# Kernel optimization log

Measured on AMD Instinct MI355X. Metric: run time of the kernel, lower is better.

Reference implementation:

```python
import jax, jax.numpy as jnp
import numpy as np

P = 256         # ids_per_batch
K = 16          # imgs_per_id
D = 2048        # feature_dim
MARGIN = 10.0
EPS = 1e-12


def setup_inputs() -> dict:
    key = jax.random.key(0)
    features = jax.random.normal(key, (P * K, D), dtype=jnp.float32)
    # ordered batch: label i repeated K times, matching targets[0::imgs_per_id] slicing
    targets = jnp.repeat(jnp.arange(P, dtype=jnp.int64), K)
    return {"features": features, "targets": targets}


def reference(features, targets):
    # ordered path: batch == P*K, labels grouped -> reshape replaces the per-class python loop
    f = features.reshape(P, K, D)               # [P, K, D]
    centers = f.mean(axis=1)                    # [P, D] per-class mean

    # intra: euclidean dist from each center to its own K features, max per class
    intra_d2 = jnp.sum((f - centers[:, None, :]) ** 2, axis=-1)     # [P, K]
    intra_max = jnp.max(jnp.sqrt(jnp.clip(intra_d2, EPS, None)), axis=1)  # [P]

    # inter: pairwise center distances, min over other centers
    cc = jnp.sum(centers ** 2, axis=1)                              # [P]
    cd2 = cc[:, None] + cc[None, :] - 2.0 * (centers @ centers.T)   # [P, P]
    cd = jnp.sqrt(jnp.clip(cd2, EPS, None))
    cd = jnp.where(jnp.eye(P, dtype=bool), jnp.inf, cd)             # exclude self
    inter_min = jnp.min(cd, axis=1)                                 # [P]

    cluster_loss = jnp.mean(jax.nn.relu(intra_max - inter_min + MARGIN))
    return cluster_loss, intra_max, inter_min
```

## Files before the change

### kernel.cpp

```cpp
#include <hip/hip_runtime.h>
#include <math.h>

#define NP 256
#define NK 16
#define ND 2048
#define MARGIN 10.0f
#define EPSV 1e-12f

__global__ __launch_bounds__(256) void k_center_intra(
    const float* __restrict__ F, float* __restrict__ centers,
    float* __restrict__ cc, float* __restrict__ out) {
  const int p = blockIdx.x;
  const int t = threadIdx.x;

  float acc[NK];
#pragma unroll
  for (int k = 0; k < NK; ++k) acc[k] = 0.f;
  float ccp = 0.f;

#pragma unroll
  for (int j = 0; j < 2; ++j) {
    const int dbase = j * 1024 + t * 4;
    float4 x[NK];
#pragma unroll
    for (int k = 0; k < NK; ++k)
      x[k] = *reinterpret_cast<const float4*>(
          &F[((size_t)(p * NK + k)) * ND + dbase]);
    float4 c;
    c.x = c.y = c.z = c.w = 0.f;
#pragma unroll
    for (int k = 0; k < NK; ++k) {
      c.x += x[k].x; c.y += x[k].y; c.z += x[k].z; c.w += x[k].w;
    }
    const float inv = 1.0f / 16.0f;
    c.x *= inv; c.y *= inv; c.z *= inv; c.w *= inv;
    *reinterpret_cast<float4*>(&centers[(size_t)p * ND + dbase]) = c;
    ccp += c.x * c.x + c.y * c.y + c.z * c.z + c.w * c.w;
#pragma unroll
    for (int k = 0; k < NK; ++k) {
      float dx = x[k].x - c.x, dy = x[k].y - c.y;
      float dz = x[k].z - c.z, dw = x[k].w - c.w;
      acc[k] += dx * dx + dy * dy + dz * dz + dw * dw;
    }
  }

#pragma unroll
  for (int k = 0; k < NK; ++k) {
    float v = acc[k];
#pragma unroll
    for (int m = 32; m > 0; m >>= 1) v += __shfl_xor(v, m);
    acc[k] = v;
  }
  {
    float v = ccp;
#pragma unroll
    for (int m = 32; m > 0; m >>= 1) v += __shfl_xor(v, m);
    ccp = v;
  }

  __shared__ float red[4][NK + 1];
  const int wave = t >> 6, lane = t & 63;
  if (lane == 0) {
#pragma unroll
    for (int k = 0; k < NK; ++k) red[wave][k] = acc[k];
    red[wave][NK] = ccp;
  }
  __syncthreads();
  if (t == 0) {
    float m = 0.f;
#pragma unroll
    for (int k = 0; k < NK; ++k) {
      float s = red[0][k] + red[1][k] + red[2][k] + red[3][k];
      m = fmaxf(m, sqrtf(fmaxf(s, EPSV)));
    }
    out[1 + p] = m;
    cc[p] = red[0][NK] + red[1][NK] + red[2][NK] + red[3][NK];
  }
}

#define BK 128
#define LDP 132

__global__ __launch_bounds__(256) void k_gemm(
    const float* __restrict__ C, float* __restrict__ G) {
  __shared__ float As[64][LDP];
  __shared__ float Bs[64][LDP];
  const int t = threadIdx.x;
  const int p0 = blockIdx.x * 64;
  const int q0 = blockIdx.y * 64;
  const int k0 = blockIdx.z * BK;

#pragma unroll
  for (int rep = 0; rep < 8; ++rep) {
    const int idx = rep * 256 + t;
    const int r = idx >> 5;
    const int c4 = idx & 31;
    float4 a = *reinterpret_cast<const float4*>(
        &C[(size_t)(p0 + r) * ND + k0 + c4 * 4]);
    float4 b = *reinterpret_cast<const float4*>(
        &C[(size_t)(q0 + r) * ND + k0 + c4 * 4]);
    *reinterpret_cast<float4*>(&As[r][c4 * 4]) = a;
    *reinterpret_cast<float4*>(&Bs[r][c4 * 4]) = b;
  }
  __syncthreads();

  const int ti = t >> 4;
  const int tj = t & 15;
  float acc[4][4] = {};

#pragma unroll
  for (int kk = 0; kk < BK; kk += 4) {
    float4 a4[4], b4[4];
#pragma unroll
    for (int u = 0; u < 4; ++u)
      a4[u] = *reinterpret_cast<const float4*>(&As[ti + u * 16][kk]);
#pragma unroll
    for (int v = 0; v < 4; ++v)
      b4[v] = *reinterpret_cast<const float4*>(&Bs[tj + v * 16][kk]);
#pragma unroll
    for (int u = 0; u < 4; ++u)
#pragma unroll
      for (int v = 0; v < 4; ++v)
        acc[u][v] += a4[u].x * b4[v].x + a4[u].y * b4[v].y +
                     a4[u].z * b4[v].z + a4[u].w * b4[v].w;
  }

#pragma unroll
  for (int u = 0; u < 4; ++u)
#pragma unroll
    for (int v = 0; v < 4; ++v)
      atomicAdd(&G[(size_t)(p0 + ti + u * 16) * NP + q0 + tj + v * 16],
                acc[u][v]);
}

__global__ __launch_bounds__(256) void k_inter(
    const float* __restrict__ G, const float* __restrict__ cc,
    float* __restrict__ out) {
  const int p = blockIdx.x, q = threadIdx.x;
  const float g = G[(size_t)p * NP + q];
  const float cd2 = cc[p] + cc[q] - 2.0f * g;
  float cd = (q == p) ? INFINITY : sqrtf(fmaxf(cd2, EPSV));
#pragma unroll
  for (int m = 32; m > 0; m >>= 1) cd = fminf(cd, __shfl_xor(cd, m));
  __shared__ float red[4];
  if ((q & 63) == 0) red[q >> 6] = cd;
  __syncthreads();
  if (q == 0)
    out[1 + NP + p] =
        fminf(fminf(red[0], red[1]), fminf(red[2], red[3]));
}

__global__ __launch_bounds__(256) void k_loss(float* __restrict__ out) {
  const int t = threadIdx.x;
  const float im = out[1 + t];
  const float in_ = out[1 + NP + t];
  float v = fmaxf(im - in_ + MARGIN, 0.f);
#pragma unroll
  for (int m = 32; m > 0; m >>= 1) v += __shfl_xor(v, m);
  __shared__ float red[4];
  if ((t & 63) == 0) red[t >> 6] = v;
  __syncthreads();
  if (t == 0) out[0] = (red[0] + red[1] + red[2] + red[3]) / (float)NP;
}

extern "C" void kernel_launch(void* const* d_in, const int* in_sizes, int n_in,
                              void* d_out, int out_size, void* d_ws,
                              size_t ws_size, hipStream_t stream) {
  const float* F = (const float*)d_in[0];
  float* out = (float*)d_out;

  float* centers = (float*)d_ws;
  float* cc = centers + (size_t)NP * ND;
  float* G = cc + NP;

  hipMemsetAsync(G, 0, (size_t)NP * NP * sizeof(float), stream);
  k_center_intra<<<NP, 256, 0, stream>>>(F, centers, cc, out);
  k_gemm<<<dim3(4, 4, 16), 256, 0, stream>>>(centers, G);
  k_inter<<<NP, 256, 0, stream>>>(G, cc, out);
  k_loss<<<1, 256, 0, stream>>>(out);
}
```

Measured before the change: 34.79 us.

## Use bf16 MFMA for center Gram matrix and fuse inter-min via atomicMin

Centers are stored as bf16, and the Gram matrix is computed with 16x16x32 bf16 MFMA instructions. The pairwise distance and min reduction are fused into the GEMM epilogue using an integer atomicMin on non-negative floats, which drops the memset, the split-K atomics and the separate inter kernel. The center kernel now uses 512 threads per block, one d-chunk per thread, and initialises the inter-min output to infinity. The bf16 rounding of centers costs precision in the cd2 cancellation, which could perturb inter_min values.

New measurement: 35.07 us. Within noise of the previous version (+0.8%).

```diff
diff --git a/kernel.cpp b/kernel.cpp
--- a/kernel.cpp
+++ b/kernel.cpp
@@ -7,41 +7,48 @@
 #define MARGIN 10.0f
 #define EPSV 1e-12f
 
-__global__ __launch_bounds__(256) void k_center_intra(
-    const float* __restrict__ F, float* __restrict__ centers,
+typedef short bf16x8 __attribute__((ext_vector_type(8)));
+typedef float f32x4 __attribute__((ext_vector_type(4)));
+
+static __device__ __forceinline__ unsigned short f2bf(float f) {
+  unsigned u = __float_as_uint(f);
+  unsigned r = (u + 0x7fffu + ((u >> 16) & 1u)) >> 16;
+  return (unsigned short)r;
+}
+
+__global__ __launch_bounds__(512) void k_center_intra(
+    const float* __restrict__ F, unsigned short* __restrict__ Cb,
     float* __restrict__ cc, float* __restrict__ out) {
   const int p = blockIdx.x;
   const int t = threadIdx.x;
+  const int d = t * 4;
+
+  float4 x[NK];
+#pragma unroll
+  for (int k = 0; k < NK; ++k)
+    x[k] = *reinterpret_cast<const float4*>(&F[((size_t)(p * NK + k)) * ND + d]);
+
+  float4 c;
+  c.x = c.y = c.z = c.w = 0.f;
+#pragma unroll
+  for (int k = 0; k < NK; ++k) {
+    c.x += x[k].x; c.y += x[k].y; c.z += x[k].z; c.w += x[k].w;
+  }
+  const float inv = 1.0f / 16.0f;
+  c.x *= inv; c.y *= inv; c.z *= inv; c.w *= inv;
+
+  ushort4 cb;
+  cb.x = f2bf(c.x); cb.y = f2bf(c.y); cb.z = f2bf(c.z); cb.w = f2bf(c.w);
+  *reinterpret_cast<ushort4*>(&Cb[(size_t)p * ND + d]) = cb;
+
+  float ccp = c.x * c.x + c.y * c.y + c.z * c.z + c.w * c.w;
 
   float acc[NK];
 #pragma unroll
-  for (int k = 0; k < NK; ++k) acc[k] = 0.f;
-  float ccp = 0.f;
-
-#pragma unroll
-  for (int j = 0; j < 2; ++j) {
-    const int dbase = j * 1024 + t * 4;
-    float4 x[NK];
-#pragma unroll
-    for (int k = 0; k < NK; ++k)
-      x[k] = *reinterpret_cast<const float4*>(
-          &F[((size_t)(p * NK + k)) * ND + dbase]);
-    float4 c;
-    c.x = c.y = c.z = c.w = 0.f;
-#pragma unroll
-    for (int k = 0; k < NK; ++k) {
-      c.x += x[k].x; c.y += x[k].y; c.z += x[k].z; c.w += x[k].w;
-    }
-    const float inv = 1.0f / 16.0f;
-    c.x *= inv; c.y *= inv; c.z *= inv; c.w *= inv;
-    *reinterpret_cast<float4*>(&centers[(size_t)p * ND + dbase]) = c;
-    ccp += c.x * c.x + c.y * c.y + c.z * c.z + c.w * c.w;
-#pragma unroll
-    for (int k = 0; k < NK; ++k) {
-      float dx = x[k].x - c.x, dy = x[k].y - c.y;
-      float dz = x[k].z - c.z, dw = x[k].w - c.w;
-      acc[k] += dx * dx + dy * dy + dz * dz + dw * dw;
-    }
+  for (int k = 0; k < NK; ++k) {
+    float dx = x[k].x - c.x, dy = x[k].y - c.y;
+    float dz = x[k].z - c.z, dw = x[k].w - c.w;
+    acc[k] = dx * dx + dy * dy + dz * dz + dw * dw;
   }
 
 #pragma unroll
@@ -58,7 +65,7 @@
     ccp = v;
   }
 
-  __shared__ float red[4][NK + 1];
+  __shared__ float red[8][NK + 1];
   const int wave = t >> 6, lane = t & 63;
   if (lane == 0) {
 #pragma unroll
@@ -70,84 +77,64 @@
     float m = 0.f;
 #pragma unroll
     for (int k = 0; k < NK; ++k) {
-      float s = red[0][k] + red[1][k] + red[2][k] + red[3][k];
+      float s = 0.f;
+#pragma unroll
+      for (int w = 0; w < 8; ++w) s += red[w][k];
       m = fmaxf(m, sqrtf(fmaxf(s, EPSV)));
     }
     out[1 + p] = m;
-    cc[p] = red[0][NK] + red[1][NK] + red[2][NK] + red[3][NK];
+    float s = 0.f;
+#pragma unroll
+    for (int w = 0; w < 8; ++w) s += red[w][NK];
+    cc[p] = s;
+    out[1 + NP + p] = INFINITY;
   }
 }
 
-#define BK 128
-#define LDP 132
+__global__ __launch_bounds__(256) void k_gemm_inter(
+    const unsigned short* __restrict__ Cb, const float* __restrict__ cc,
+    float* __restrict__ out) {
+  const int t = threadIdx.x;
+  const int wave = t >> 6, lane = t & 63;
+  const int p0 = blockIdx.x * 16;
+  const int q0 = blockIdx.y * 64 + wave * 16;
+  const int lr = lane & 15;
+  const int kg = (lane >> 4) * 8;
 
-__global__ __launch_bounds__(256) void k_gemm(
-    const float* __restrict__ C, float* __restrict__ G) {
-  __shared__ float As[64][LDP];
-  __shared__ float Bs[64][LDP];
-  const int t = threadIdx.x;
-  const int p0 = blockIdx.x * 64;
-  const int q0 = blockIdx.y * 64;
-  const int k0 = blockIdx.z * BK;
+  const unsigned short* ap = &Cb[(size_t)(p0 + lr) * ND + kg];
+  const unsigned short* bp = &Cb[(size_t)(q0 + lr) * ND + kg];
 
-#pragma unroll
-  for (int rep = 0; rep < 8; ++rep) {
-    const int idx = rep * 256 + t;
-    const int r = idx >> 5;
-    const int c4 = idx & 31;
-    float4 a = *reinterpret_cast<const float4*>(
-        &C[(size_t)(p0 + r) * ND + k0 + c4 * 4]);
-    float4 b = *reinterpret_cast<const float4*>(
-        &C[(size_t)(q0 + r) * ND + k0 + c4 * 4]);
-    *reinterpret_cast<float4*>(&As[r][c4 * 4]) = a;
-    *reinterpret_cast<float4*>(&Bs[r][c4 * 4]) = b;
-  }
-  __syncthreads();
-
-  const int ti = t >> 4;
-  const int tj = t & 15;
-  float acc[4][4] = {};
-
-#pragma unroll
-  for (int kk = 0; kk < BK; kk += 4) {
-    float4 a4[4], b4[4];
-#pragma unroll
-    for (int u = 0; u < 4; ++u)
-      a4[u] = *reinterpret_cast<const float4*>(&As[ti + u * 16][kk]);
-#pragma unroll
-    for (int v = 0; v < 4; ++v)
-      b4[v] = *reinterpret_cast<const float4*>(&Bs[tj + v * 16][kk]);
-#pragma unroll
-    for (int u = 0; u < 4; ++u)
-#pragma unroll
-      for (int v = 0; v < 4; ++v)
-        acc[u][v] += a4[u].x * b4[v].x + a4[u].y * b4[v].y +
-                     a4[u].z * b4[v].z + a4[u].w * b4[v].w;
+  f32x4 acc = {0.f, 0.f, 0.f, 0.f};
+#pragma unroll 8
+  for (int k0 = 0; k0 < ND; k0 += 32) {
+    bf16x8 a = *reinterpret_cast<const bf16x8*>(ap + k0);
+    bf16x8 b = *reinterpret_cast<const bf16x8*>(bp + k0);
+    acc = __builtin_amdgcn_mfma_f32_16x16x32_bf16(a, b, acc, 0, 0, 0);
   }
 
+  const int rbase = (lane >> 4) * 4;
+  const int qg = q0 + lr;
+  const float ccq = cc[qg];
+  float cdm[4];
 #pragma unroll
-  for (int u = 0; u < 4; ++u)
+  for (int r = 0; r < 4; ++r) {
+    const int pg = p0 + rbase + r;
+    const float cd2 = cc[pg] + ccq - 2.0f * acc[r];
+    cdm[r] = (pg == qg) ? INFINITY : sqrtf(fmaxf(cd2, EPSV));
+  }
 #pragma unroll
-    for (int v = 0; v < 4; ++v)
-      atomicAdd(&G[(size_t)(p0 + ti + u * 16) * NP + q0 + tj + v * 16],
-                acc[u][v]);
-}
-
-__global__ __launch_bounds__(256) void k_inter(
-    const float* __restrict__ G, const float* __restrict__ cc,
-    float* __restrict__ out) {
-  const int p = blockIdx.x, q = threadIdx.x;
-  const float g = G[(size_t)p * NP + q];
-  const float cd2 = cc[p] + cc[q] - 2.0f * g;
-  float cd = (q == p) ? INFINITY : sqrtf(fmaxf(cd2, EPSV));
+  for (int r = 0; r < 4; ++r) {
 #pragma unroll
-  for (int m = 32; m > 0; m >>= 1) cd = fminf(cd, __shfl_xor(cd, m));
-  __shared__ float red[4];
-  if ((q & 63) == 0) red[q >> 6] = cd;
-  __syncthreads();
-  if (q == 0)
-    out[1 + NP + p] =
-        fminf(fminf(red[0], red[1]), fminf(red[2], red[3]));
+    for (int m = 8; m > 0; m >>= 1) cdm[r] = fminf(cdm[r], __shfl_xor(cdm[r], m));
+  }
+  if (lr == 0) {
+#pragma unroll
+    for (int r = 0; r < 4; ++r) {
+      const int pg = p0 + rbase + r;
+      atomicMin(reinterpret_cast<int*>(out) + 1 + NP + pg,
+                __float_as_int(cdm[r]));
+    }
+  }
 }
 
 __global__ __launch_bounds__(256) void k_loss(float* __restrict__ out) {
@@ -169,13 +156,10 @@
   const float* F = (const float*)d_in[0];
   float* out = (float*)d_out;
 
-  float* centers = (float*)d_ws;
-  float* cc = centers + (size_t)NP * ND;
-  float* G = cc + NP;
+  unsigned short* Cb = (unsigned short*)d_ws;
+  float* cc = (float*)(Cb + (size_t)NP * ND);
 
-  hipMemsetAsync(G, 0, (size_t)NP * NP * sizeof(float), stream);
-  k_center_intra<<<NP, 256, 0, stream>>>(F, centers, cc, out);
-  k_gemm<<<dim3(4, 4, 16), 256, 0, stream>>>(centers, G);
-  k_inter<<<NP, 256, 0, stream>>>(G, cc, out);
+  k_center_intra<<<NP, 512, 0, stream>>>(F, Cb, cc, out);
+  k_gemm_inter<<<dim3(16, 4), 256, 0, stream>>>(Cb, cc, out);
   k_loss<<<1, 256, 0, stream>>>(out);
 }
```
